# Kernel optimization log

Hardware: AMD Instinct MI355X
Metric: run time of the kernel (lower is better)

The kernel has to match this reference:

```python
import jax, jax.numpy as jnp
import numpy as np

N = 50000      # nodes
E = 800000     # edges (avg degree 16)
H = 128        # hidden_dim
MAXDEG = 200   # max_degree


def setup_inputs() -> dict:
    key = jax.random.key(0)
    ks = jax.random.split(key, 16)
    rn = lambda k, shape: jax.random.normal(k, shape, jnp.float32) * 0.05
    return {
        'x': jax.random.normal(ks[0], (N, 1), jnp.float32),
        'edge_index': jax.random.randint(ks[1], (2, E), 0, N),
        'W_enc': rn(ks[2], (H, 1)), 'b_enc': rn(ks[3], (H,)),
        'deg_emb': rn(ks[4], (MAXDEG, H)),
        'W1l': rn(ks[5], (H, H)), 'b1l': jnp.zeros((H,), jnp.float32), 'W1r': rn(ks[6], (H, H)),
        'W2l': rn(ks[7], (H, H)), 'b2l': jnp.zeros((H,), jnp.float32), 'W2r': rn(ks[8], (H, H)),
        'W3l': rn(ks[9], (H, H)), 'b3l': jnp.zeros((H,), jnp.float32), 'W3r': rn(ks[10], (H, H)),
        'Wh1': rn(ks[11], (H // 2, H)), 'bh1': jnp.zeros((H // 2,), jnp.float32),
        'Wh2': rn(ks[12], (1, H // 2)), 'bh2': jnp.zeros((1,), jnp.float32),
    }


def _sage(h, src, dst, n, Wl, bl, Wr):
    # PyG SAGEConv (aggr='mean'): lin_l(mean_j x_j) + lin_r(x_i); lin_r has no bias.
    msg = h[src]                                           # [E,H] gather
    s = jax.ops.segment_sum(msg, dst, num_segments=n)      # [N,H]
    cnt = jax.ops.segment_sum(jnp.ones((src.shape[0],), h.dtype), dst, num_segments=n)
    agg = s / jnp.maximum(cnt, 1.0)[:, None]               # zero-in-degree -> 0
    return agg @ Wl.T + bl + h @ Wr.T


def reference(x, edge_index, W_enc, b_enc, deg_emb, W1l, b1l, W1r,
              W2l, b2l, W2r, W3l, b3l, W3r, Wh1, bh1, Wh2, bh2):
    n = x.shape[0]
    src, dst = edge_index[0], edge_index[1]
    # degree(edge_index[0], num_nodes): out-degree per node, clamped
    degs = jax.ops.segment_sum(jnp.ones((src.shape[0],), jnp.float32), src, num_segments=n)
    degs = jnp.clip(degs, 0, MAXDEG - 1).astype(jnp.int32)
    h = jax.nn.relu(x @ W_enc.T + b_enc + deg_emb[degs])
    h1 = jax.nn.relu(_sage(h, src, dst, n, W1l, b1l, W1r))
    h2 = jax.nn.relu(_sage(h1, src, dst, n, W2l, b2l, W2r)) + h1
    h3 = jax.nn.relu(_sage(h2, src, dst, n, W3l, b3l, W3r)) + h2
    z = jax.nn.relu(h3 @ Wh1.T + bh1)   # dropout inactive at eval
    scores = (z @ Wh2.T + bh2)[:, 0][None, :]   # [1, N]
    return scores
```

## Files before the change

### kernel.cpp

```cpp
#include <hip/hip_runtime.h>


#define HDIM 128
#define NB 256
#define MAXBUK 512
#define SCH 4096

typedef __attribute__((ext_vector_type(8))) short short8;
typedef __attribute__((ext_vector_type(4))) float f32x4;

__device__ inline float bf2f(unsigned short u) {
    union { unsigned int u; float f; } t; t.u = (unsigned int)u << 16; return t.f;
}
__device__ inline unsigned short f2bf(float f) {
    union { float f; unsigned int u; } t; t.f = f;
    unsigned int u = t.u;
    return (unsigned short)((u + 0x7FFFu + ((u >> 16) & 1u)) >> 16);
}


__global__ __launch_bounds__(256) void binhist_kernel(const int* __restrict__ src,
                                                      const int* __restrict__ dst,
                                                      int* __restrict__ hist,
                                                      int E, int nbuk, int ec) {
    __shared__ int hD[MAXBUK], hS[MAXBUK];
    const int tid = threadIdx.x, bid = blockIdx.x;
    for (int i = tid; i < nbuk; i += 256) { hD[i] = 0; hS[i] = 0; }
    __syncthreads();
    const int s0 = bid * ec, s1 = min(E, s0 + ec);
    for (int e = s0 + tid; e < s1; e += 256) {
        atomicAdd(&hD[dst[e] >> 7], 1);
        atomicAdd(&hS[src[e] >> 7], 1);
    }
    __syncthreads();
    for (int i = tid; i < nbuk; i += 256) {
        hist[(size_t)i * NB + bid] = hD[i];
        hist[(size_t)(nbuk + i) * NB + bid] = hS[i];
    }
}


__global__ __launch_bounds__(256) void hscan1_kernel(const int* __restrict__ a,
                                                     int* __restrict__ bsum, int L) {
    __shared__ int shw[4];
    const int tid = threadIdx.x;
    const int base = blockIdx.x * SCH + tid * 16;
    int s = 0;
#pragma unroll
    for (int j = 0; j < 16; ++j) { int i = base + j; if (i < L) s += a[i]; }
#pragma unroll
    for (int off = 32; off > 0; off >>= 1) s += __shfl_down(s, off, 64);
    if ((tid & 63) == 0) shw[tid >> 6] = s;
    __syncthreads();
    if (tid == 0) bsum[blockIdx.x] = shw[0] + shw[1] + shw[2] + shw[3];
}

__global__ void hscan2_kernel(int* __restrict__ bsum, int nb) {
    int lane = threadIdx.x;
    int v = (lane < nb) ? bsum[lane] : 0;
    int orig = v;
#pragma unroll
    for (int off = 1; off < 64; off <<= 1) {
        int t = __shfl_up(v, off, 64);
        if (lane >= off) v += t;
    }
    if (lane < nb) bsum[lane] = v - orig;
}

__global__ __launch_bounds__(256) void hscan3_kernel(const int* __restrict__ a,
                                                     const int* __restrict__ bsum,
                                                     int* __restrict__ out, int L) {
    __shared__ int shw[4];
    const int tid = threadIdx.x;
    const int lane = tid & 63;
    const int w = tid >> 6;
    const int base = blockIdx.x * SCH + tid * 16;
    int v[16];
    int s = 0;
#pragma unroll
    for (int j = 0; j < 16; ++j) {
        int i = base + j;
        v[j] = (i < L) ? a[i] : 0;
        s += v[j];
    }
    int incl = s;
#pragma unroll
    for (int off = 1; off < 64; off <<= 1) {
        int t = __shfl_up(incl, off, 64);
        if (lane >= off) incl += t;
    }
    if (lane == 63) shw[w] = incl;
    __syncthreads();
    int woff = 0;
#pragma unroll
    for (int j = 0; j < 4; ++j) if (j < w) woff += shw[j];
    int pfx = bsum[blockIdx.x] + woff + incl - s;
#pragma unroll
    for (int j = 0; j < 16; ++j) {
        int i = base + j;
        if (i < L) out[i] = pfx;
        pfx += v[j];
    }
}


__global__ __launch_bounds__(256) void binscatter_kernel(const int* __restrict__ src,
                                                         const int* __restrict__ dst,
                                                         const int* __restrict__ scanned,
                                                         unsigned int* __restrict__ binD,
                                                         unsigned char* __restrict__ binS,
                                                         int E, int nbuk, int ec) {
    __shared__ int curD[MAXBUK], curS[MAXBUK];
    const int tid = threadIdx.x, bid = blockIdx.x;
    for (int i = tid; i < nbuk; i += 256) {
        curD[i] = scanned[(size_t)i * NB + bid];
        curS[i] = scanned[(size_t)(nbuk + i) * NB + bid] - E;
    }
    __syncthreads();
    const int s0 = bid * ec, s1 = min(E, s0 + ec);
    for (int e = s0 + tid; e < s1; e += 256) {
        int s = src[e], d = dst[e];
        int pd = atomicAdd(&curD[d >> 7], 1);
        binD[pd] = (unsigned int)s | ((unsigned int)(d & 127) << 16);
        int ps = atomicAdd(&curS[s >> 7], 1);
        binS[ps] = (unsigned char)(s & 127);
    }
}


__global__ __launch_bounds__(256) void finalize_kernel(const unsigned int* __restrict__ binD,
                                                       const unsigned char* __restrict__ binS,
                                                       const int* __restrict__ scanned,
                                                       unsigned short* __restrict__ csr,
                                                       int* __restrict__ rowptr,
                                                       int* __restrict__ outdeg,
                                                       int E, int n, int nbuk) {
    __shared__ int cntD[128], cur[128], cntS[128];
    const int b = blockIdx.x, tid = threadIdx.x;
    if (tid < 128) { cntD[tid] = 0; cntS[tid] = 0; }
    __syncthreads();
    const int s0 = scanned[(size_t)b * NB];
    const int s1 = (b == nbuk - 1) ? E : scanned[(size_t)(b + 1) * NB];
    const int t0 = scanned[(size_t)(nbuk + b) * NB] - E;
    const int t1 = (b == nbuk - 1) ? E : scanned[(size_t)(nbuk + b + 1) * NB] - E;
    for (int e = s0 + tid; e < s1; e += 256) atomicAdd(&cntD[(binD[e] >> 16) & 127], 1);
    for (int e = t0 + tid; e < t1; e += 256) atomicAdd(&cntS[binS[e]], 1);
    __syncthreads();
    if (tid < 128) cur[tid] = cntD[tid];
    __syncthreads();
    for (int off = 1; off < 128; off <<= 1) {
        int t = (tid < 128 && tid >= off) ? cur[tid - off] : 0;
        __syncthreads();
        if (tid < 128) cur[tid] += t;
        __syncthreads();
    }
    if (tid < 128) {
        int ex = cur[tid] - cntD[tid];
        int node = b * 128 + tid;
        if (node < n) { rowptr[node] = s0 + ex; outdeg[node] = cntS[tid]; }
        cur[tid] = ex;
    }
    __syncthreads();
    for (int e = s0 + tid; e < s1; e += 256) {
        unsigned int p = binD[e];
        int pos = atomicAdd(&cur[(p >> 16) & 127], 1);
        csr[s0 + pos] = (unsigned short)(p & 0xFFFFu);
    }
    if (b == 0 && tid == 0) rowptr[n] = E;
}


__global__ void wconv_kernel(const float* __restrict__ W1l, const float* __restrict__ W1r,
                             const float* __restrict__ W2l, const float* __restrict__ W2r,
                             const float* __restrict__ W3l, const float* __restrict__ W3r,
                             const float* __restrict__ Wh1,
                             unsigned short* __restrict__ out) {
    int idx = blockIdx.x * 256 + threadIdx.x;
    const float* s;
    int o;
    if (idx < 98304) {
        int m = idx >> 14; o = idx & 16383;
        switch (m) {
            case 0: s = W1l; break; case 1: s = W1r; break;
            case 2: s = W2l; break; case 3: s = W2r; break;
            case 4: s = W3l; break; default: s = W3r; break;
        }
    } else {
        s = Wh1; o = idx - 98304;
    }
    out[idx] = f2bf(s[o]);
}


__global__ void encoder_kernel(const float* __restrict__ x, const float* __restrict__ Wenc,
                               const float* __restrict__ benc, const float* __restrict__ demb,
                               const int* __restrict__ outdeg,
                               unsigned short* __restrict__ h, int n) {
    int idx = blockIdx.x * blockDim.x + threadIdx.x;
    if (idx >= n * 16) return;
    int i = idx >> 4, g = idx & 15;
    int d = outdeg[i]; if (d > 199) d = 199;
    float xv = x[i];
    const float* wp = Wenc + g * 8;
    const float* bp = benc + g * 8;
    const float* ep = demb + (size_t)d * HDIM + g * 8;
    short8 o;
#pragma unroll
    for (int j = 0; j < 8; ++j)
        o[j] = (short)f2bf(fmaxf(xv * wp[j] + bp[j] + ep[j], 0.f));
    *(short8*)(h + (size_t)i * HDIM + g * 8) = o;
}


__global__ __launch_bounds__(256) void aggregate_kernel(const unsigned short* __restrict__ hin,
                                                        const int* __restrict__ row_ptr,
                                                        const unsigned short* __restrict__ csr,
                                                        unsigned short* __restrict__ agg, int n) {
    const int tid = threadIdx.x;
    const int i = blockIdx.x * 16 + (tid >> 4);
    if (i >= n) return;
    const int l16 = tid & 15;
    const int beg = row_ptr[i], end = row_ptr[i + 1];
    float a[8] = {};
    int e = beg;
    for (; e + 3 < end; e += 4) {
        int s0 = csr[e], s1 = csr[e + 1], s2 = csr[e + 2], s3 = csr[e + 3];
        short8 v0 = *(const short8*)(hin + (size_t)s0 * HDIM + l16 * 8);
        short8 v1 = *(const short8*)(hin + (size_t)s1 * HDIM + l16 * 8);
        short8 v2 = *(const short8*)(hin + (size_t)s2 * HDIM + l16 * 8);
        short8 v3 = *(const short8*)(hin + (size_t)s3 * HDIM + l16 * 8);
#pragma unroll
        for (int j = 0; j < 8; ++j)
            a[j] += (bf2f((unsigned short)v0[j]) + bf2f((unsigned short)v1[j]))
                  + (bf2f((unsigned short)v2[j]) + bf2f((unsigned short)v3[j]));
    }
    for (; e < end; ++e) {
        int s0 = csr[e];
        short8 v0 = *(const short8*)(hin + (size_t)s0 * HDIM + l16 * 8);
#pragma unroll
        for (int j = 0; j < 8; ++j) a[j] += bf2f((unsigned short)v0[j]);
    }
    float inv = 1.f / fmaxf((float)(end - beg), 1.f);
    short8 o;
#pragma unroll
    for (int j = 0; j < 8; ++j) o[j] = (short)f2bf(a[j] * inv);
    *(short8*)(agg + (size_t)i * HDIM + l16 * 8) = o;
}


template <bool RES>
__global__ __launch_bounds__(256) void gemm_mfma(const unsigned short* __restrict__ agg,
                                                 const unsigned short* __restrict__ hin,
                                                 const unsigned short* __restrict__ Wl,
                                                 const unsigned short* __restrict__ Wr,
                                                 const float* __restrict__ bias,
                                                 unsigned short* __restrict__ outBf, int n) {
    const int t = threadIdx.x;
    const int l = t & 63;
    const int wv = t >> 6;
    const int l16 = l & 15;
    const int q = l >> 4;
    const int row0 = blockIdx.x * 128 + wv * 32;
    const int node0 = min(row0 + l16, n - 1);
    const int node1 = min(row0 + 16 + l16, n - 1);

    const unsigned short* wlp = Wl + (size_t)l16 * HDIM + q * 8;
    const unsigned short* wrp = Wr + (size_t)l16 * HDIM + q * 8;
    const unsigned short* ap0 = agg + (size_t)node0 * HDIM + q * 8;
    const unsigned short* hp0 = hin + (size_t)node0 * HDIM + q * 8;
    const unsigned short* ap1 = agg + (size_t)node1 * HDIM + q * 8;
    const unsigned short* hp1 = hin + (size_t)node1 * HDIM + q * 8;

    f32x4 acc[2][8] = {};
#pragma unroll
    for (int k0 = 0; k0 < 128; k0 += 32) {
        short8 xa0 = *(const short8*)(ap0 + k0);
        short8 xh0 = *(const short8*)(hp0 + k0);
        short8 xa1 = *(const short8*)(ap1 + k0);
        short8 xh1 = *(const short8*)(hp1 + k0);
#pragma unroll
        for (int ct = 0; ct < 8; ++ct) {
            short8 bl = *(const short8*)(wlp + (size_t)ct * 16 * HDIM + k0);
            short8 br = *(const short8*)(wrp + (size_t)ct * 16 * HDIM + k0);
            acc[0][ct] = __builtin_amdgcn_mfma_f32_16x16x32_bf16(bl, xa0, acc[0][ct], 0, 0, 0);
            acc[0][ct] = __builtin_amdgcn_mfma_f32_16x16x32_bf16(br, xh0, acc[0][ct], 0, 0, 0);
            acc[1][ct] = __builtin_amdgcn_mfma_f32_16x16x32_bf16(bl, xa1, acc[1][ct], 0, 0, 0);
            acc[1][ct] = __builtin_amdgcn_mfma_f32_16x16x32_bf16(br, xh1, acc[1][ct], 0, 0, 0);
        }
    }

#pragma unroll
    for (int ng = 0; ng < 2; ++ng) {
        int node = row0 + ng * 16 + l16;
        if (node >= n) continue;
        int cnode = min(node, n - 1);
#pragma unroll
        for (int ct = 0; ct < 8; ++ct) {
            const int c0 = ct * 16 + q * 4;
            float4 bv = *(const float4*)(bias + c0);
            float v0 = fmaxf(acc[ng][ct][0] + bv.x, 0.f);
            float v1 = fmaxf(acc[ng][ct][1] + bv.y, 0.f);
            float v2 = fmaxf(acc[ng][ct][2] + bv.z, 0.f);
            float v3 = fmaxf(acc[ng][ct][3] + bv.w, 0.f);
            if (RES) {
                const unsigned short* rp = hin + (size_t)cnode * HDIM + c0;
                uint2 rv = *(const uint2*)rp;
                v0 += bf2f((unsigned short)(rv.x & 0xFFFF));
                v1 += bf2f((unsigned short)(rv.x >> 16));
                v2 += bf2f((unsigned short)(rv.y & 0xFFFF));
                v3 += bf2f((unsigned short)(rv.y >> 16));
            }
            unsigned int o0 = (unsigned int)f2bf(v0) | ((unsigned int)f2bf(v1) << 16);
            unsigned int o1 = (unsigned int)f2bf(v2) | ((unsigned int)f2bf(v3) << 16);
            uint2 o; o.x = o0; o.y = o1;
            *(uint2*)(outBf + (size_t)node * HDIM + c0) = o;
        }
    }
}


__global__ __launch_bounds__(256) void head_mfma(const unsigned short* __restrict__ h3,
                                                 const unsigned short* __restrict__ Wh1b,
                                                 const float* __restrict__ bh1,
                                                 const float* __restrict__ Wh2,
                                                 const float* __restrict__ bh2,
                                                 float* __restrict__ scores, int n) {
    const int t = threadIdx.x;
    const int l = t & 63;
    const int wv = t >> 6;
    const int l16 = l & 15;
    const int q = l >> 4;
    const int row0 = blockIdx.x * 256 + wv * 64;

    const unsigned short* whp = Wh1b + (size_t)l16 * HDIM + q * 8;

    f32x4 acc[4][4] = {};
#pragma unroll
    for (int k0 = 0; k0 < 128; k0 += 32) {
        short8 xf[4];
#pragma unroll
        for (int ng = 0; ng < 4; ++ng) {
            int node = min(row0 + ng * 16 + l16, n - 1);
            xf[ng] = *(const short8*)(h3 + (size_t)node * HDIM + q * 8 + k0);
        }
#pragma unroll
        for (int ct = 0; ct < 4; ++ct) {
            short8 wf = *(const short8*)(whp + (size_t)ct * 16 * HDIM + k0);
#pragma unroll
            for (int ng = 0; ng < 4; ++ng)
                acc[ng][ct] = __builtin_amdgcn_mfma_f32_16x16x32_bf16(wf, xf[ng], acc[ng][ct], 0, 0, 0);
        }
    }

    const float bh2v = bh2[0];
#pragma unroll
    for (int ng = 0; ng < 4; ++ng) {
        float p = 0.f;
#pragma unroll
        for (int ct = 0; ct < 4; ++ct) {
            const int c0 = ct * 16 + q * 4;
            float4 b1 = *(const float4*)(bh1 + c0);
            float4 w2 = *(const float4*)(Wh2 + c0);
            p += fmaxf(acc[ng][ct][0] + b1.x, 0.f) * w2.x;
            p += fmaxf(acc[ng][ct][1] + b1.y, 0.f) * w2.y;
            p += fmaxf(acc[ng][ct][2] + b1.z, 0.f) * w2.z;
            p += fmaxf(acc[ng][ct][3] + b1.w, 0.f) * w2.w;
        }
        p += __shfl_xor(p, 16, 64);
        p += __shfl_xor(p, 32, 64);
        int node = row0 + ng * 16 + l16;
        if (q == 0 && node < n) scores[node] = p + bh2v;
    }
}


extern "C" void kernel_launch(void* const* d_in, const int* in_sizes, int n_in,
                              void* d_out, int out_size, void* d_ws, size_t ws_size,
                              hipStream_t stream) {
    const int N = in_sizes[0];
    const int E = in_sizes[1] / 2;
    const int H = HDIM;

    const float* x    = (const float*)d_in[0];
    const int*   ei   = (const int*)d_in[1];
    const int*   src  = ei;
    const int*   dst  = ei + E;
    const float* Wenc = (const float*)d_in[2];
    const float* benc = (const float*)d_in[3];
    const float* demb = (const float*)d_in[4];
    const float* W1l  = (const float*)d_in[5];
    const float* b1l  = (const float*)d_in[6];
    const float* W1r  = (const float*)d_in[7];
    const float* W2l  = (const float*)d_in[8];
    const float* b2l  = (const float*)d_in[9];
    const float* W2r  = (const float*)d_in[10];
    const float* W3l  = (const float*)d_in[11];
    const float* b3l  = (const float*)d_in[12];
    const float* W3r  = (const float*)d_in[13];
    const float* Wh1  = (const float*)d_in[14];
    const float* bh1  = (const float*)d_in[15];
    const float* Wh2  = (const float*)d_in[16];
    const float* bh2  = (const float*)d_in[17];

    const int nbuk = (N + 127) >> 7;
    const int L    = 2 * nbuk * NB;
    const int nbk  = (L + SCH - 1) / SCH;
    const int ec   = (E + NB - 1) / NB;

    size_t off = 0;
    char* base = (char*)d_ws;
    auto carve = [&](size_t bytes) -> char* {
        char* p = base + off;
        off += (bytes + 255) & ~(size_t)255;
        return p;
    };
    unsigned short* bufA = (unsigned short*)carve((size_t)N * H * 2);
    unsigned short* bufB = (unsigned short*)carve((size_t)N * H * 2);
    unsigned short* bufC = (unsigned short*)carve((size_t)N * H * 2);
    unsigned short* csr  = (unsigned short*)carve((size_t)E * 2);
    int*   rowptr  = (int*)carve((size_t)(N + 1) * 4);
    int*   outdeg  = (int*)carve((size_t)N * 4);
    int*   bsum    = (int*)carve(4096);
    int*   hist    = (int*)carve((size_t)L * 4);
    int*   scanned = (int*)carve((size_t)L * 4);
    unsigned int*  binD = (unsigned int*)carve((size_t)E * 4);
    unsigned char* binS = (unsigned char*)carve((size_t)E);
    unsigned short* Wb  = (unsigned short*)carve((size_t)(6 * H * H + 64 * H) * 2);
    (void)ws_size; (void)n_in; (void)out_size;

    unsigned short* W1lb = Wb;
    unsigned short* W1rb = Wb + 1 * H * H;
    unsigned short* W2lb = Wb + 2 * H * H;
    unsigned short* W2rb = Wb + 3 * H * H;
    unsigned short* W3lb = Wb + 4 * H * H;
    unsigned short* W3rb = Wb + 5 * H * H;
    unsigned short* Wh1b = Wb + 6 * H * H;

    binhist_kernel<<<NB, 256, 0, stream>>>(src, dst, hist, E, nbuk, ec);
    hscan1_kernel<<<nbk, 256, 0, stream>>>(hist, bsum, L);
    hscan2_kernel<<<1, 64, 0, stream>>>(bsum, nbk);
    hscan3_kernel<<<nbk, 256, 0, stream>>>(hist, bsum, scanned, L);
    binscatter_kernel<<<NB, 256, 0, stream>>>(src, dst, scanned, binD, binS, E, nbuk, ec);
    finalize_kernel<<<nbuk, 256, 0, stream>>>(binD, binS, scanned, csr, rowptr, outdeg,
                                              E, N, nbuk);

    wconv_kernel<<<(6 * H * H + 64 * H) / 256, 256, 0, stream>>>(
        W1l, W1r, W2l, W2r, W3l, W3r, Wh1, Wb);

    encoder_kernel<<<((size_t)N * 16 + 255) / 256, 256, 0, stream>>>(
        x, Wenc, benc, demb, outdeg, bufA, N);

    const int gAgg  = (N + 15) / 16;
    const int gGemm = (N + 127) / 128;
    const int gHead = (N + 255) / 256;

    aggregate_kernel<<<gAgg, 256, 0, stream>>>(bufA, rowptr, csr, bufB, N);
    gemm_mfma<false><<<gGemm, 256, 0, stream>>>(bufB, bufA, W1lb, W1rb, b1l, bufC, N);

    aggregate_kernel<<<gAgg, 256, 0, stream>>>(bufC, rowptr, csr, bufB, N);
    gemm_mfma<true><<<gGemm, 256, 0, stream>>>(bufB, bufC, W2lb, W2rb, b2l, bufA, N);

    aggregate_kernel<<<gAgg, 256, 0, stream>>>(bufA, rowptr, csr, bufB, N);
    gemm_mfma<true><<<gGemm, 256, 0, stream>>>(bufB, bufA, W3lb, W3rb, b3l, bufC, N);

    head_mfma<<<gHead, 256, 0, stream>>>(bufC, Wh1b, bh1, Wh2, bh2, (float*)d_out, N);
}
```

Measured before the change: 225.0 us.

## Fuse mean aggregation, SAGE GEMM, and output head into one kernel per layer

```diff
diff --git a/kernel.cpp b/kernel.cpp
--- a/kernel.cpp
+++ b/kernel.cpp
@@ -212,165 +212,166 @@
 }
 
 
-__global__ __launch_bounds__(256) void aggregate_kernel(const unsigned short* __restrict__ hin,
-                                                        const int* __restrict__ row_ptr,
-                                                        const unsigned short* __restrict__ csr,
-                                                        unsigned short* __restrict__ agg, int n) {
-    const int tid = threadIdx.x;
-    const int i = blockIdx.x * 16 + (tid >> 4);
-    if (i >= n) return;
-    const int l16 = tid & 15;
-    const int beg = row_ptr[i], end = row_ptr[i + 1];
-    float a[8] = {};
-    int e = beg;
-    for (; e + 3 < end; e += 4) {
-        int s0 = csr[e], s1 = csr[e + 1], s2 = csr[e + 2], s3 = csr[e + 3];
-        short8 v0 = *(const short8*)(hin + (size_t)s0 * HDIM + l16 * 8);
-        short8 v1 = *(const short8*)(hin + (size_t)s1 * HDIM + l16 * 8);
-        short8 v2 = *(const short8*)(hin + (size_t)s2 * HDIM + l16 * 8);
-        short8 v3 = *(const short8*)(hin + (size_t)s3 * HDIM + l16 * 8);
-#pragma unroll
-        for (int j = 0; j < 8; ++j)
-            a[j] += (bf2f((unsigned short)v0[j]) + bf2f((unsigned short)v1[j]))
-                  + (bf2f((unsigned short)v2[j]) + bf2f((unsigned short)v3[j]));
-    }
-    for (; e < end; ++e) {
-        int s0 = csr[e];
-        short8 v0 = *(const short8*)(hin + (size_t)s0 * HDIM + l16 * 8);
-#pragma unroll
-        for (int j = 0; j < 8; ++j) a[j] += bf2f((unsigned short)v0[j]);
-    }
-    float inv = 1.f / fmaxf((float)(end - beg), 1.f);
-    short8 o;
-#pragma unroll
-    for (int j = 0; j < 8; ++j) o[j] = (short)f2bf(a[j] * inv);
-    *(short8*)(agg + (size_t)i * HDIM + l16 * 8) = o;
-}
-
-
-template <bool RES>
-__global__ __launch_bounds__(256) void gemm_mfma(const unsigned short* __restrict__ agg,
-                                                 const unsigned short* __restrict__ hin,
-                                                 const unsigned short* __restrict__ Wl,
-                                                 const unsigned short* __restrict__ Wr,
-                                                 const float* __restrict__ bias,
-                                                 unsigned short* __restrict__ outBf, int n) {
+template <bool RES, bool HEAD>
+__global__ __launch_bounds__(512) void sage_fused(const unsigned short* __restrict__ hin,
+                                                  const int* __restrict__ row_ptr,
+                                                  const unsigned short* __restrict__ csr,
+                                                  const unsigned short* __restrict__ Wl,
+                                                  const unsigned short* __restrict__ Wr,
+                                                  const float* __restrict__ bias,
+                                                  unsigned short* __restrict__ outBf,
+                                                  const unsigned short* __restrict__ Wh1b,
+                                                  const float* __restrict__ bh1,
+                                                  const float* __restrict__ Wh2,
+                                                  const float* __restrict__ bh2,
+                                                  float* __restrict__ scores, int n) {
+    __shared__ unsigned short sAgg[128][128];
     const int t = threadIdx.x;
+    const int row0b = blockIdx.x * 128;
+
+    {
+        const int g = t >> 4;
+        const int lg = t & 15;
+        for (int jj = 0; jj < 4; ++jj) {
+            const int j = g * 4 + jj;
+            const int node = row0b + j;
+            float a[8] = {};
+            if (node < n) {
+                const int beg = row_ptr[node];
+                const int end = row_ptr[node + 1];
+                for (int e = beg; e < end; e += 8) {
+                    short8 v[8];
+#pragma unroll
+                    for (int u = 0; u < 8; ++u) {
+                        int ee = e + u; if (ee > end - 1) ee = end - 1;
+                        int sidx = csr[ee];
+                        v[u] = *(const short8*)(hin + (size_t)sidx * HDIM + lg * 8);
+                    }
+#pragma unroll
+                    for (int u = 0; u < 8; ++u) {
+                        if (e + u < end) {
+#pragma unroll
+                            for (int k = 0; k < 8; ++k)
+                                a[k] += bf2f((unsigned short)v[u][k]);
+                        }
+                    }
+                }
+                float inv = 1.f / fmaxf((float)(end - beg), 1.f);
+#pragma unroll
+                for (int k = 0; k < 8; ++k) a[k] *= inv;
+            }
+            short8 o;
+#pragma unroll
+            for (int k = 0; k < 8; ++k) o[k] = (short)f2bf(a[k]);
+            *(short8*)(&sAgg[j][(lg ^ (j & 7)) * 8]) = o;
+        }
+    }
+    __syncthreads();
+
     const int l = t & 63;
     const int wv = t >> 6;
     const int l16 = l & 15;
     const int q = l >> 4;
-    const int row0 = blockIdx.x * 128 + wv * 32;
-    const int node0 = min(row0 + l16, n - 1);
-    const int node1 = min(row0 + 16 + l16, n - 1);
+    const int lrow = wv * 16 + l16;
+    const int node = row0b + lrow;
+    const int cnode = min(node, n - 1);
 
     const unsigned short* wlp = Wl + (size_t)l16 * HDIM + q * 8;
     const unsigned short* wrp = Wr + (size_t)l16 * HDIM + q * 8;
-    const unsigned short* ap0 = agg + (size_t)node0 * HDIM + q * 8;
-    const unsigned short* hp0 = hin + (size_t)node0 * HDIM + q * 8;
-    const unsigned short* ap1 = agg + (size_t)node1 * HDIM + q * 8;
-    const unsigned short* hp1 = hin + (size_t)node1 * HDIM + q * 8;
-
-    f32x4 acc[2][8] = {};
+    const unsigned short* hp = hin + (size_t)cnode * HDIM + q * 8;
+
+    f32x4 acc[8] = {};
 #pragma unroll
     for (int k0 = 0; k0 < 128; k0 += 32) {
-        short8 xa0 = *(const short8*)(ap0 + k0);
-        short8 xh0 = *(const short8*)(hp0 + k0);
-        short8 xa1 = *(const short8*)(ap1 + k0);
-        short8 xh1 = *(const short8*)(hp1 + k0);
+        const int ch = q + (k0 >> 3);
+        short8 xa = *(const short8*)(&sAgg[lrow][(ch ^ (lrow & 7)) * 8]);
+        short8 xh = *(const short8*)(hp + k0);
 #pragma unroll
         for (int ct = 0; ct < 8; ++ct) {
             short8 bl = *(const short8*)(wlp + (size_t)ct * 16 * HDIM + k0);
             short8 br = *(const short8*)(wrp + (size_t)ct * 16 * HDIM + k0);
-            acc[0][ct] = __builtin_amdgcn_mfma_f32_16x16x32_bf16(bl, xa0, acc[0][ct], 0, 0, 0);
-            acc[0][ct] = __builtin_amdgcn_mfma_f32_16x16x32_bf16(br, xh0, acc[0][ct], 0, 0, 0);
-            acc[1][ct] = __builtin_amdgcn_mfma_f32_16x16x32_bf16(bl, xa1, acc[1][ct], 0, 0, 0);
-            acc[1][ct] = __builtin_amdgcn_mfma_f32_16x16x32_bf16(br, xh1, acc[1][ct], 0, 0, 0);
-        }
-    }
-
-#pragma unroll
-    for (int ng = 0; ng < 2; ++ng) {
-        int node = row0 + ng * 16 + l16;
-        if (node >= n) continue;
-        int cnode = min(node, n - 1);
-#pragma unroll
-        for (int ct = 0; ct < 8; ++ct) {
-            const int c0 = ct * 16 + q * 4;
-            float4 bv = *(const float4*)(bias + c0);
-            float v0 = fmaxf(acc[ng][ct][0] + bv.x, 0.f);
-            float v1 = fmaxf(acc[ng][ct][1] + bv.y, 0.f);
-            float v2 = fmaxf(acc[ng][ct][2] + bv.z, 0.f);
-            float v3 = fmaxf(acc[ng][ct][3] + bv.w, 0.f);
-            if (RES) {
-                const unsigned short* rp = hin + (size_t)cnode * HDIM + c0;
-                uint2 rv = *(const uint2*)rp;
-                v0 += bf2f((unsigned short)(rv.x & 0xFFFF));
-                v1 += bf2f((unsigned short)(rv.x >> 16));
-                v2 += bf2f((unsigned short)(rv.y & 0xFFFF));
-                v3 += bf2f((unsigned short)(rv.y >> 16));
+            acc[ct] = __builtin_amdgcn_mfma_f32_16x16x32_bf16(bl, xa, acc[ct], 0, 0, 0);
+            acc[ct] = __builtin_amdgcn_mfma_f32_16x16x32_bf16(br, xh, acc[ct], 0, 0, 0);
+        }
+    }
+
+    if (!HEAD) {
+        if (node < n) {
+#pragma unroll
+            for (int ct = 0; ct < 8; ++ct) {
+                const int c0 = ct * 16 + q * 4;
+                float4 bv = *(const float4*)(bias + c0);
+                float v0 = fmaxf(acc[ct][0] + bv.x, 0.f);
+                float v1 = fmaxf(acc[ct][1] + bv.y, 0.f);
+                float v2 = fmaxf(acc[ct][2] + bv.z, 0.f);
+                float v3 = fmaxf(acc[ct][3] + bv.w, 0.f);
+                if (RES) {
+                    uint2 rv = *(const uint2*)(hin + (size_t)cnode * HDIM + c0);
+                    v0 += bf2f((unsigned short)(rv.x & 0xFFFF));
+                    v1 += bf2f((unsigned short)(rv.x >> 16));
+                    v2 += bf2f((unsigned short)(rv.y & 0xFFFF));
+                    v3 += bf2f((unsigned short)(rv.y >> 16));
+                }
+                unsigned int o0 = (unsigned int)f2bf(v0) | ((unsigned int)f2bf(v1) << 16);
+                unsigned int o1 = (unsigned int)f2bf(v2) | ((unsigned int)f2bf(v3) << 16);
+                uint2 o; o.x = o0; o.y = o1;
+                *(uint2*)(outBf + (size_t)node * HDIM + c0) = o;
             }
-            unsigned int o0 = (unsigned int)f2bf(v0) | ((unsigned int)f2bf(v1) << 16);
-            unsigned int o1 = (unsigned int)f2bf(v2) | ((unsigned int)f2bf(v3) << 16);
-            uint2 o; o.x = o0; o.y = o1;
-            *(uint2*)(outBf + (size_t)node * HDIM + c0) = o;
-        }
-    }
-}
-
-
-__global__ __launch_bounds__(256) void head_mfma(const unsigned short* __restrict__ h3,
-                                                 const unsigned short* __restrict__ Wh1b,
-                                                 const float* __restrict__ bh1,
-                                                 const float* __restrict__ Wh2,
-                                                 const float* __restrict__ bh2,
-                                                 float* __restrict__ scores, int n) {
-    const int t = threadIdx.x;
-    const int l = t & 63;
-    const int wv = t >> 6;
-    const int l16 = l & 15;
-    const int q = l >> 4;
-    const int row0 = blockIdx.x * 256 + wv * 64;
+        }
+        return;
+    }
+
+#pragma unroll
+    for (int ct = 0; ct < 8; ++ct) {
+        const int c0 = ct * 16 + q * 4;
+        float4 bv = *(const float4*)(bias + c0);
+        float v0 = fmaxf(acc[ct][0] + bv.x, 0.f);
+        float v1 = fmaxf(acc[ct][1] + bv.y, 0.f);
+        float v2 = fmaxf(acc[ct][2] + bv.z, 0.f);
+        float v3 = fmaxf(acc[ct][3] + bv.w, 0.f);
+        if (RES) {
+            uint2 rv = *(const uint2*)(hin + (size_t)cnode * HDIM + c0);
+            v0 += bf2f((unsigned short)(rv.x & 0xFFFF));
+            v1 += bf2f((unsigned short)(rv.x >> 16));
+            v2 += bf2f((unsigned short)(rv.y & 0xFFFF));
+            v3 += bf2f((unsigned short)(rv.y >> 16));
+        }
+        const int ch = 2 * ct + (q >> 1);
+        unsigned short* p = &sAgg[lrow][((ch ^ (lrow & 7)) * 8) + (q & 1) * 4];
+        unsigned int o0 = (unsigned int)f2bf(v0) | ((unsigned int)f2bf(v1) << 16);
+        unsigned int o1 = (unsigned int)f2bf(v2) | ((unsigned int)f2bf(v3) << 16);
+        uint2 o; o.x = o0; o.y = o1;
+        *(uint2*)p = o;
+    }
 
     const unsigned short* whp = Wh1b + (size_t)l16 * HDIM + q * 8;
-
-    f32x4 acc[4][4] = {};
+    f32x4 hacc[4] = {};
 #pragma unroll
     for (int k0 = 0; k0 < 128; k0 += 32) {
-        short8 xf[4];
-#pragma unroll
-        for (int ng = 0; ng < 4; ++ng) {
-            int node = min(row0 + ng * 16 + l16, n - 1);
-            xf[ng] = *(const short8*)(h3 + (size_t)node * HDIM + q * 8 + k0);
-        }
+        const int ch = q + (k0 >> 3);
+        short8 xf = *(const short8*)(&sAgg[lrow][(ch ^ (lrow & 7)) * 8]);
 #pragma unroll
         for (int ct = 0; ct < 4; ++ct) {
             short8 wf = *(const short8*)(whp + (size_t)ct * 16 * HDIM + k0);
-#pragma unroll
-            for (int ng = 0; ng < 4; ++ng)
-                acc[ng][ct] = __builtin_amdgcn_mfma_f32_16x16x32_bf16(wf, xf[ng], acc[ng][ct], 0, 0, 0);
+            hacc[ct] = __builtin_amdgcn_mfma_f32_16x16x32_bf16(wf, xf, hacc[ct], 0, 0, 0);
         }
     }
 
     const float bh2v = bh2[0];
-#pragma unroll
-    for (int ng = 0; ng < 4; ++ng) {
-        float p = 0.f;
-#pragma unroll
-        for (int ct = 0; ct < 4; ++ct) {
-            const int c0 = ct * 16 + q * 4;
-            float4 b1 = *(const float4*)(bh1 + c0);
-            float4 w2 = *(const float4*)(Wh2 + c0);
-            p += fmaxf(acc[ng][ct][0] + b1.x, 0.f) * w2.x;
-            p += fmaxf(acc[ng][ct][1] + b1.y, 0.f) * w2.y;
-            p += fmaxf(acc[ng][ct][2] + b1.z, 0.f) * w2.z;
-            p += fmaxf(acc[ng][ct][3] + b1.w, 0.f) * w2.w;
-        }
-        p += __shfl_xor(p, 16, 64);
-        p += __shfl_xor(p, 32, 64);
-        int node = row0 + ng * 16 + l16;
-        if (q == 0 && node < n) scores[node] = p + bh2v;
-    }
+    float p = 0.f;
+#pragma unroll
+    for (int ct = 0; ct < 4; ++ct) {
+        const int c0 = ct * 16 + q * 4;
+        float4 b1 = *(const float4*)(bh1 + c0);
+        float4 w2 = *(const float4*)(Wh2 + c0);
+        p += fmaxf(hacc[ct][0] + b1.x, 0.f) * w2.x;
+        p += fmaxf(hacc[ct][1] + b1.y, 0.f) * w2.y;
+        p += fmaxf(hacc[ct][2] + b1.z, 0.f) * w2.z;
+        p += fmaxf(hacc[ct][3] + b1.w, 0.f) * w2.w;
+    }
+    p += __shfl_xor(p, 16, 64);
+    p += __shfl_xor(p, 32, 64);
+    if (q == 0 && node < n) scores[node] = p + bh2v;
 }
 
 
@@ -416,7 +417,6 @@
     };
     unsigned short* bufA = (unsigned short*)carve((size_t)N * H * 2);
     unsigned short* bufB = (unsigned short*)carve((size_t)N * H * 2);
-    unsigned short* bufC = (unsigned short*)carve((size_t)N * H * 2);
     unsigned short* csr  = (unsigned short*)carve((size_t)E * 2);
     int*   rowptr  = (int*)carve((size_t)(N + 1) * 4);
     int*   outdeg  = (int*)carve((size_t)N * 4);
@@ -450,18 +450,15 @@
     encoder_kernel<<<((size_t)N * 16 + 255) / 256, 256, 0, stream>>>(
         x, Wenc, benc, demb, outdeg, bufA, N);
 
-    const int gAgg  = (N + 15) / 16;
-    const int gGemm = (N + 127) / 128;
-    const int gHead = (N + 255) / 256;
-
-    aggregate_kernel<<<gAgg, 256, 0, stream>>>(bufA, rowptr, csr, bufB, N);
-    gemm_mfma<false><<<gGemm, 256, 0, stream>>>(bufB, bufA, W1lb, W1rb, b1l, bufC, N);
-
-    aggregate_kernel<<<gAgg, 256, 0, stream>>>(bufC, rowptr, csr, bufB, N);
-    gemm_mfma<true><<<gGemm, 256, 0, stream>>>(bufB, bufC, W2lb, W2rb, b2l, bufA, N);
-
-    aggregate_kernel<<<gAgg, 256, 0, stream>>>(bufA, rowptr, csr, bufB, N);
-    gemm_mfma<true><<<gGemm, 256, 0, stream>>>(bufB, bufA, W3lb, W3rb, b3l, bufC, N);
-
-    head_mfma<<<gHead, 256, 0, stream>>>(bufC, Wh1b, bh1, Wh2, bh2, (float*)d_out, N);
-}
+    const int gF = (N + 127) / 128;
+
+    sage_fused<false, false><<<gF, 512, 0, stream>>>(bufA, rowptr, csr, W1lb, W1rb, b1l,
+                                                     bufB, nullptr, nullptr, nullptr,
+                                                     nullptr, nullptr, N);
+    sage_fused<true, false><<<gF, 512, 0, stream>>>(bufB, rowptr, csr, W2lb, W2rb, b2l,
+                                                    bufA, nullptr, nullptr, nullptr,
+                                                    nullptr, nullptr, N);
+    sage_fused<true, true><<<gF, 512, 0, stream>>>(bufA, rowptr, csr, W3lb, W3rb, b3l,
+                                                   nullptr, Wh1b, bh1, Wh2, bh2,
+                                                   (float*)d_out, N);
+}
```

Result: slower. 264.7 us (+17.6%).
